# Optimization experiments

Hardware: AMD Instinct MI355X
Metric: run time of the kernel (lower is better)

The kernel has to match this reference:

```python
import jax, jax.numpy as jnp
import numpy as np

B, N, C_IN, D, K = 4, 512, 256, 256, 20


def setup_inputs() -> dict:
    key = jax.random.key(0)
    ks = jax.random.split(key, 6)
    s_in = 1.0 / np.sqrt(C_IN)
    return {
        "x": jax.random.normal(ks[0], (B, N, C_IN), dtype=jnp.float32),
        "edge_index": jnp.zeros((2, 4), dtype=jnp.int64),
        "batch": jnp.zeros((B * N,), dtype=jnp.int64),
        "W_l": jax.random.uniform(ks[1], (D, C_IN), jnp.float32, -s_in, s_in),
        "b_l": jax.random.uniform(ks[2], (D,), jnp.float32, -s_in, s_in),
        "W_r": jax.random.uniform(ks[3], (D, C_IN), jnp.float32, -s_in, s_in),
        "b_r": jax.random.uniform(ks[4], (D,), jnp.float32, -s_in, s_in),
        "att": jax.random.normal(ks[5], (1, D), dtype=jnp.float32) * 0.1,
    }


def reference(x, edge_index, batch, W_l, b_l, W_r, b_r, att):
    b, n, _ = x.shape
    k = K
    # linear projections -> [b, n, d]
    x_l = jnp.einsum("bnc,dc->bnd", x, W_l) + b_l
    x_r = jnp.einsum("bnc,dc->bnd", x, W_r) + b_r
    # pairwise additive attention: [b, n, n, d]
    pair = x_l[:, :, None, :] + x_r[:, None, :, :]
    pair = jnp.where(pair >= 0, pair, 0.2 * pair)  # leaky_relu(0.2)
    alpha = jnp.einsum("bijd,d->bij", pair, att[0])  # [b, n, n]
    alpha = jnp.nan_to_num(alpha, nan=0.0, posinf=0.0, neginf=0.0)
    # knn reduction: topk over last dim
    attention, indices = jax.lax.top_k(alpha, k)  # [b, n, k]
    attention = jax.nn.softmax(attention, axis=-1).reshape(-1)  # [b*n*k]
    # edge index construction with per-batch node offsets
    offset = (jnp.arange(b, dtype=indices.dtype) * n)[:, None]  # [b, 1]
    index_i = jnp.repeat(jnp.arange(n, dtype=indices.dtype), k)[None, :] + offset
    index_j = indices.reshape(b, n * k) + offset
    new_edge_index = jnp.stack([index_i.reshape(-1), index_j.reshape(-1)], axis=0)
    # dropout is identity in eval mode; learn_sys=False -> return directly
    return new_edge_index, attention
```

## Files before the change

### kernel.cpp

```cpp
#include <hip/hip_runtime.h>
#include <math.h>


__global__ __launch_bounds__(256) void k_transpose(const float* __restrict__ Wl,
                                                   const float* __restrict__ Wr,
                                                   float* __restrict__ WtL,
                                                   float* __restrict__ WtR) {
    const int d = blockIdx.x, c = threadIdx.x;
    if (blockIdx.y == 0) WtL[c * 256 + d] = Wl[d * 256 + c];
    else                 WtR[c * 256 + d] = Wr[d * 256 + c];
}

__global__ __launch_bounds__(512, 4) void k_proj(const float* __restrict__ x,
        const float* __restrict__ WtL, const float* __restrict__ WtR,
        const float* __restrict__ bl, const float* __restrict__ br,
        const float* __restrict__ att,
        float* __restrict__ XL, float* __restrict__ XRt,
        float* __restrict__ Av, float* __restrict__ Bv) {
    __shared__ __align__(16) float xst[256 * 12];
    __shared__ __align__(16) float mrg[3 * 4096];
    __shared__ __align__(16) float srs[8 * 256];
    const int tid = threadIdx.x;
    const int dq = tid & 63;
    const int rq = (tid >> 6) & 1;
    const int ch = tid >> 7;
    const int R = blockIdx.x * 8;
    const int b = R >> 9, jr0 = R & 511;

    {
        const float4 xv = ((const float4*)(x + (size_t)R * 256))[tid];
        const int r = tid >> 6;
        const int c4 = (tid & 63) * 4;
        xst[(c4 + 0) * 12 + r] = xv.x;
        xst[(c4 + 1) * 12 + r] = xv.y;
        xst[(c4 + 2) * 12 + r] = xv.z;
        xst[(c4 + 3) * 12 + r] = xv.w;
    }
    __syncthreads();

    float aL[4][4], aR[4][4];
#pragma unroll
    for (int r = 0; r < 4; ++r)
#pragma unroll
        for (int k = 0; k < 4; ++k) { aL[r][k] = 0.f; aR[r][k] = 0.f; }

    const int c0 = ch * 64;
    const float* WLp = WtL + (size_t)c0 * 256 + dq * 4;
    const float* WRp = WtR + (size_t)c0 * 256 + dq * 4;
#pragma unroll 4
    for (int cc = 0; cc < 64; ++cc) {
        const float4 wl = *(const float4*)(WLp + (size_t)cc * 256);
        const float4 wr = *(const float4*)(WRp + (size_t)cc * 256);
        const float4 xv = *(const float4*)&xst[(c0 + cc) * 12 + rq * 4];
#define PROJ_R(r, XS)                                  \
        aL[r][0] = fmaf(XS, wl.x, aL[r][0]);           \
        aL[r][1] = fmaf(XS, wl.y, aL[r][1]);           \
        aL[r][2] = fmaf(XS, wl.z, aL[r][2]);           \
        aL[r][3] = fmaf(XS, wl.w, aL[r][3]);           \
        aR[r][0] = fmaf(XS, wr.x, aR[r][0]);           \
        aR[r][1] = fmaf(XS, wr.y, aR[r][1]);           \
        aR[r][2] = fmaf(XS, wr.z, aR[r][2]);           \
        aR[r][3] = fmaf(XS, wr.w, aR[r][3]);
        PROJ_R(0, xv.x)
        PROJ_R(1, xv.y)
        PROJ_R(2, xv.z)
        PROJ_R(3, xv.w)
#undef PROJ_R
    }

    if (ch > 0) {
        float* m = &mrg[(ch - 1) * 4096];
#pragma unroll
        for (int r = 0; r < 4; ++r) {
            const int r8 = rq * 4 + r;
            *(float4*)&m[(r8 * 2 + 0) * 256 + dq * 4] = make_float4(aL[r][0], aL[r][1], aL[r][2], aL[r][3]);
            *(float4*)&m[(r8 * 2 + 1) * 256 + dq * 4] = make_float4(aR[r][0], aR[r][1], aR[r][2], aR[r][3]);
        }
    }
    __syncthreads();

    float pa[4], pb[4];
    if (ch == 0) {
        const float4 bl4 = *(const float4*)&bl[dq * 4];
        const float4 br4 = *(const float4*)&br[dq * 4];
        const float4 at4 = *(const float4*)&att[dq * 4];
#pragma unroll
        for (int r = 0; r < 4; ++r) {
            const int r8 = rq * 4 + r;
            const float4 mL0 = *(const float4*)&mrg[(r8 * 2 + 0) * 256 + dq * 4];
            const float4 mL1 = *(const float4*)&mrg[4096 + (r8 * 2 + 0) * 256 + dq * 4];
            const float4 mL2 = *(const float4*)&mrg[8192 + (r8 * 2 + 0) * 256 + dq * 4];
            const float4 mR0 = *(const float4*)&mrg[(r8 * 2 + 1) * 256 + dq * 4];
            const float4 mR1 = *(const float4*)&mrg[4096 + (r8 * 2 + 1) * 256 + dq * 4];
            const float4 mR2 = *(const float4*)&mrg[8192 + (r8 * 2 + 1) * 256 + dq * 4];
            float4 sl, sr;
            sl.x = aL[r][0] + mL0.x + mL1.x + mL2.x + bl4.x;
            sl.y = aL[r][1] + mL0.y + mL1.y + mL2.y + bl4.y;
            sl.z = aL[r][2] + mL0.z + mL1.z + mL2.z + bl4.z;
            sl.w = aL[r][3] + mL0.w + mL1.w + mL2.w + bl4.w;
            sr.x = aR[r][0] + mR0.x + mR1.x + mR2.x + br4.x;
            sr.y = aR[r][1] + mR0.y + mR1.y + mR2.y + br4.y;
            sr.z = aR[r][2] + mR0.z + mR1.z + mR2.z + br4.z;
            sr.w = aR[r][3] + mR0.w + mR1.w + mR2.w + br4.w;
            *(float4*)&XL[(size_t)(R + r8) * 256 + dq * 4] = sl;
            *(float4*)&srs[r8 * 256 + dq * 4] = sr;
            pa[r] = at4.x * sl.x + at4.y * sl.y + at4.z * sl.z + at4.w * sl.w;
            pb[r] = at4.x * sr.x + at4.y * sr.y + at4.z * sr.z + at4.w * sr.w;
        }
    }
    __syncthreads();

    {
        const int d = tid >> 1;
        const int half = tid & 1;
        float4 o;
        o.x = srs[(half * 4 + 0) * 256 + d];
        o.y = srs[(half * 4 + 1) * 256 + d];
        o.z = srs[(half * 4 + 2) * 256 + d];
        o.w = srs[(half * 4 + 3) * 256 + d];
        *(float4*)&XRt[((size_t)(b * 256 + d)) * 512 + jr0 + half * 4] = o;
    }

    if (ch == 0) {
#pragma unroll
        for (int r = 0; r < 4; ++r) {
#pragma unroll
            for (int off = 32; off; off >>= 1) {
                pa[r] += __shfl_xor(pa[r], off);
                pb[r] += __shfl_xor(pb[r], off);
            }
        }
        if (dq == 0) {
#pragma unroll
            for (int r = 0; r < 4; ++r) {
                Av[R + rq * 4 + r] = pa[r];
                Bv[R + rq * 4 + r] = pb[r];
            }
        }
    }
}

__global__ __launch_bounds__(512, 2) void k_pair_topk(const float* __restrict__ XL,
        const float* __restrict__ XRt, const float* __restrict__ Av,
        const float* __restrict__ Bv, const float* __restrict__ att,
        float* __restrict__ out) {
    __shared__ __align__(16) float xls[8 * 256];
    __shared__ __align__(16) float atts[256];
    __shared__ __align__(16) float mrg[4 * 4096];
    const int tid = threadIdx.x;
    const int jc = tid & 127;
    const int h = tid >> 7;
    const int g = blockIdx.x;
    const int R = g * 8, b = R >> 9;

    ((float4*)xls)[tid] = ((const float4*)(XL + (size_t)R * 256))[tid];
    if (tid < 64) ((float4*)atts)[tid] = ((const float4*)att)[tid];
    __syncthreads();

    const int dbase = h * 64;
    const float* __restrict__ xrp = XRt + (size_t)b * 131072 + (size_t)dbase * 512 + jc * 4;

    float acc[8][4];
#pragma unroll
    for (int i = 0; i < 8; ++i)
#pragma unroll
        for (int c = 0; c < 4; ++c) acc[i][c] = 0.f;

    float4 bufA[8], bufB[8];
#pragma unroll
    for (int dd = 0; dd < 8; ++dd) bufA[dd] = *(const float4*)(xrp + (size_t)dd * 512);

#pragma unroll
    for (int ch = 0; ch < 8; ++ch) {
        const float4* cur = (ch & 1) ? bufB : bufA;
        float4* nxt = (ch & 1) ? bufA : bufB;
        if (ch < 7) {
            const float* p = xrp + (size_t)(ch + 1) * 8 * 512;
#pragma unroll
            for (int dd = 0; dd < 8; ++dd) nxt[dd] = *(const float4*)(p + (size_t)dd * 512);
        }
        const int d0 = dbase + ch * 8;
        const float4 at0 = *(const float4*)&atts[d0];
        const float4 at1 = *(const float4*)&atts[d0 + 4];
#pragma unroll
        for (int i = 0; i < 8; ++i) {
            const float4 xa = *(const float4*)&xls[i * 256 + d0];
            const float4 xb = *(const float4*)&xls[i * 256 + d0 + 4];
#define PSTEP(XLC, ATC, XR4)                                       \
            acc[i][0] = fmaf(ATC, fabsf(XLC + XR4.x), acc[i][0]);   \
            acc[i][1] = fmaf(ATC, fabsf(XLC + XR4.y), acc[i][1]);   \
            acc[i][2] = fmaf(ATC, fabsf(XLC + XR4.z), acc[i][2]);   \
            acc[i][3] = fmaf(ATC, fabsf(XLC + XR4.w), acc[i][3]);
            PSTEP(xa.x, at0.x, cur[0])
            PSTEP(xa.y, at0.y, cur[1])
            PSTEP(xa.z, at0.z, cur[2])
            PSTEP(xa.w, at0.w, cur[3])
            PSTEP(xb.x, at1.x, cur[4])
            PSTEP(xb.y, at1.y, cur[5])
            PSTEP(xb.z, at1.z, cur[6])
            PSTEP(xb.w, at1.w, cur[7])
#undef PSTEP
        }
    }

    {
        float* m = &mrg[h * 4096];
#pragma unroll
        for (int i = 0; i < 8; ++i)
            *(float4*)&m[i * 512 + jc * 4] = make_float4(acc[i][0], acc[i][1], acc[i][2], acc[i][3]);
    }
    __syncthreads();

    const int lane = tid & 63;
    const int i = tid >> 6;
    const float Ai = Av[R + i];
    const float* __restrict__ bvp = Bv + b * 512;
    const float* __restrict__ mr = &mrg[i * 512];
    float v[8];
#pragma unroll
    for (int t = 0; t < 8; ++t) {
        const int j = t * 64 + lane;
        float s = mr[j];
        s += mr[4096 + j];
        s += mr[8192 + j];
        s += mr[12288 + j];
        float a = fmaf(0.4f, s, 0.6f * (Ai + bvp[j]));
        if (!isfinite(a)) a = 0.f;
        v[t] = a;
    }

    float myval = 0.f, mmax = 0.f;
    int myidx = 0;
    for (int sel = 0; sel < 20; ++sel) {
        float bv = v[0]; int bt = 0;
#pragma unroll
        for (int t = 1; t < 8; ++t) { if (v[t] > bv) { bv = v[t]; bt = t; } }
        int bj = bt * 64 + lane;
#pragma unroll
        for (int off = 32; off; off >>= 1) {
            const float ov = __shfl_xor(bv, off);
            const int   oj = __shfl_xor(bj, off);
            if (ov > bv || (ov == bv && oj < bj)) { bv = ov; bj = oj; }
        }
        if (sel == 0) mmax = bv;
        if (lane == sel) { myval = bv; myidx = bj; }
        if ((bj & 63) == lane) {
            const int bt2 = bj >> 6;
#pragma unroll
            for (int t = 0; t < 8; ++t) if (t == bt2) v[t] = -INFINITY;
        }
    }
    const float e = (lane < 20) ? expf(myval - mmax) : 0.f;
    float s = e;
#pragma unroll
    for (int off = 32; off; off >>= 1) s += __shfl_xor(s, off);
    if (lane < 20) {
        const int row = R + i;
        const int base = row * 20 + lane;
        out[base] = (float)row;
        out[40960 + base] = (float)(b * 512 + myidx);
        out[81920 + base] = e / s;
    }
}

extern "C" void kernel_launch(void* const* d_in, const int* in_sizes, int n_in,
                              void* d_out, int out_size, void* d_ws, size_t ws_size,
                              hipStream_t stream) {
    const float* x   = (const float*)d_in[0];
    const float* Wl  = (const float*)d_in[3];
    const float* bl  = (const float*)d_in[4];
    const float* Wr  = (const float*)d_in[5];
    const float* br  = (const float*)d_in[6];
    const float* att = (const float*)d_in[7];

    float* ws  = (float*)d_ws;
    float* WtL = ws;
    float* WtR = ws + 65536;
    float* XL  = ws + 1048576;
    float* XRt = ws + 1572864;
    float* Av  = ws + 2097152;
    float* Bv  = ws + 2099200;
    float* out = (float*)d_out;

    k_transpose<<<dim3(256, 2), dim3(256), 0, stream>>>(Wl, Wr, WtL, WtR);
    k_proj<<<dim3(256), dim3(512), 0, stream>>>(x, WtL, WtR, bl, br, att, XL, XRt, Av, Bv);
    k_pair_topk<<<dim3(256), dim3(512), 0, stream>>>(XL, XRt, Av, Bv, att, out);
}
```

Baseline: 115.4 us.

## Fuse projection and pairwise top-k kernels via cooperative grid sync

Merges the projection kernel and the pairwise-attention/top-k kernel into one cooperative kernel separated by a grid-wide barrier. XL now stays in shared memory instead of going through global memory, and shared buffers are aliased into one union array. This removes one kernel launch and the XL global round trip. In exchange it adds a grid sync, drops occupancy hints for the projection phase to 2 blocks per CU, and depends on all 256 blocks being co-resident.

```diff
diff --git a/kernel.cpp b/kernel.cpp
--- a/kernel.cpp
+++ b/kernel.cpp
@@ -1,5 +1,8 @@
 #include <hip/hip_runtime.h>
+#include <hip/hip_cooperative_groups.h>
 #include <math.h>
+
+namespace cg = cooperative_groups;
 
 
 __global__ __launch_bounds__(256) void k_transpose(const float* __restrict__ Wl,
@@ -11,255 +14,255 @@
     else                 WtR[c * 256 + d] = Wr[d * 256 + c];
 }
 
-__global__ __launch_bounds__(512, 4) void k_proj(const float* __restrict__ x,
+__global__ __launch_bounds__(512, 2) void k_fused(const float* __restrict__ x,
         const float* __restrict__ WtL, const float* __restrict__ WtR,
         const float* __restrict__ bl, const float* __restrict__ br,
         const float* __restrict__ att,
-        float* __restrict__ XL, float* __restrict__ XRt,
-        float* __restrict__ Av, float* __restrict__ Bv) {
-    __shared__ __align__(16) float xst[256 * 12];
-    __shared__ __align__(16) float mrg[3 * 4096];
-    __shared__ __align__(16) float srs[8 * 256];
-    const int tid = threadIdx.x;
-    const int dq = tid & 63;
-    const int rq = (tid >> 6) & 1;
-    const int ch = tid >> 7;
-    const int R = blockIdx.x * 8;
-    const int b = R >> 9, jr0 = R & 511;
-
-    {
-        const float4 xv = ((const float4*)(x + (size_t)R * 256))[tid];
-        const int r = tid >> 6;
-        const int c4 = (tid & 63) * 4;
-        xst[(c4 + 0) * 12 + r] = xv.x;
-        xst[(c4 + 1) * 12 + r] = xv.y;
-        xst[(c4 + 2) * 12 + r] = xv.z;
-        xst[(c4 + 3) * 12 + r] = xv.w;
-    }
-    __syncthreads();
-
-    float aL[4][4], aR[4][4];
-#pragma unroll
-    for (int r = 0; r < 4; ++r)
-#pragma unroll
-        for (int k = 0; k < 4; ++k) { aL[r][k] = 0.f; aR[r][k] = 0.f; }
-
-    const int c0 = ch * 64;
-    const float* WLp = WtL + (size_t)c0 * 256 + dq * 4;
-    const float* WRp = WtR + (size_t)c0 * 256 + dq * 4;
-#pragma unroll 4
-    for (int cc = 0; cc < 64; ++cc) {
-        const float4 wl = *(const float4*)(WLp + (size_t)cc * 256);
-        const float4 wr = *(const float4*)(WRp + (size_t)cc * 256);
-        const float4 xv = *(const float4*)&xst[(c0 + cc) * 12 + rq * 4];
-#define PROJ_R(r, XS)                                  \
-        aL[r][0] = fmaf(XS, wl.x, aL[r][0]);           \
-        aL[r][1] = fmaf(XS, wl.y, aL[r][1]);           \
-        aL[r][2] = fmaf(XS, wl.z, aL[r][2]);           \
-        aL[r][3] = fmaf(XS, wl.w, aL[r][3]);           \
-        aR[r][0] = fmaf(XS, wr.x, aR[r][0]);           \
-        aR[r][1] = fmaf(XS, wr.y, aR[r][1]);           \
-        aR[r][2] = fmaf(XS, wr.z, aR[r][2]);           \
-        aR[r][3] = fmaf(XS, wr.w, aR[r][3]);
-        PROJ_R(0, xv.x)
-        PROJ_R(1, xv.y)
-        PROJ_R(2, xv.z)
-        PROJ_R(3, xv.w)
-#undef PROJ_R
-    }
-
-    if (ch > 0) {
-        float* m = &mrg[(ch - 1) * 4096];
-#pragma unroll
-        for (int r = 0; r < 4; ++r) {
-            const int r8 = rq * 4 + r;
-            *(float4*)&m[(r8 * 2 + 0) * 256 + dq * 4] = make_float4(aL[r][0], aL[r][1], aL[r][2], aL[r][3]);
-            *(float4*)&m[(r8 * 2 + 1) * 256 + dq * 4] = make_float4(aR[r][0], aR[r][1], aR[r][2], aR[r][3]);
-        }
-    }
-    __syncthreads();
-
-    float pa[4], pb[4];
-    if (ch == 0) {
-        const float4 bl4 = *(const float4*)&bl[dq * 4];
-        const float4 br4 = *(const float4*)&br[dq * 4];
-        const float4 at4 = *(const float4*)&att[dq * 4];
-#pragma unroll
-        for (int r = 0; r < 4; ++r) {
-            const int r8 = rq * 4 + r;
-            const float4 mL0 = *(const float4*)&mrg[(r8 * 2 + 0) * 256 + dq * 4];
-            const float4 mL1 = *(const float4*)&mrg[4096 + (r8 * 2 + 0) * 256 + dq * 4];
-            const float4 mL2 = *(const float4*)&mrg[8192 + (r8 * 2 + 0) * 256 + dq * 4];
-            const float4 mR0 = *(const float4*)&mrg[(r8 * 2 + 1) * 256 + dq * 4];
-            const float4 mR1 = *(const float4*)&mrg[4096 + (r8 * 2 + 1) * 256 + dq * 4];
-            const float4 mR2 = *(const float4*)&mrg[8192 + (r8 * 2 + 1) * 256 + dq * 4];
-            float4 sl, sr;
-            sl.x = aL[r][0] + mL0.x + mL1.x + mL2.x + bl4.x;
-            sl.y = aL[r][1] + mL0.y + mL1.y + mL2.y + bl4.y;
-            sl.z = aL[r][2] + mL0.z + mL1.z + mL2.z + bl4.z;
-            sl.w = aL[r][3] + mL0.w + mL1.w + mL2.w + bl4.w;
-            sr.x = aR[r][0] + mR0.x + mR1.x + mR2.x + br4.x;
-            sr.y = aR[r][1] + mR0.y + mR1.y + mR2.y + br4.y;
-            sr.z = aR[r][2] + mR0.z + mR1.z + mR2.z + br4.z;
-            sr.w = aR[r][3] + mR0.w + mR1.w + mR2.w + br4.w;
-            *(float4*)&XL[(size_t)(R + r8) * 256 + dq * 4] = sl;
-            *(float4*)&srs[r8 * 256 + dq * 4] = sr;
-            pa[r] = at4.x * sl.x + at4.y * sl.y + at4.z * sl.z + at4.w * sl.w;
-            pb[r] = at4.x * sr.x + at4.y * sr.y + at4.z * sr.z + at4.w * sr.w;
-        }
-    }
-    __syncthreads();
-
-    {
-        const int d = tid >> 1;
-        const int half = tid & 1;
-        float4 o;
-        o.x = srs[(half * 4 + 0) * 256 + d];
-        o.y = srs[(half * 4 + 1) * 256 + d];
-        o.z = srs[(half * 4 + 2) * 256 + d];
-        o.w = srs[(half * 4 + 3) * 256 + d];
-        *(float4*)&XRt[((size_t)(b * 256 + d)) * 512 + jr0 + half * 4] = o;
-    }
-
-    if (ch == 0) {
-#pragma unroll
-        for (int r = 0; r < 4; ++r) {
-#pragma unroll
-            for (int off = 32; off; off >>= 1) {
-                pa[r] += __shfl_xor(pa[r], off);
-                pb[r] += __shfl_xor(pb[r], off);
-            }
-        }
-        if (dq == 0) {
-#pragma unroll
-            for (int r = 0; r < 4; ++r) {
-                Av[R + rq * 4 + r] = pa[r];
-                Bv[R + rq * 4 + r] = pb[r];
-            }
-        }
-    }
-}
-
-__global__ __launch_bounds__(512, 2) void k_pair_topk(const float* __restrict__ XL,
-        const float* __restrict__ XRt, const float* __restrict__ Av,
-        const float* __restrict__ Bv, const float* __restrict__ att,
+        float* __restrict__ XRt, float* __restrict__ Av, float* __restrict__ Bv,
         float* __restrict__ out) {
     __shared__ __align__(16) float xls[8 * 256];
     __shared__ __align__(16) float atts[256];
-    __shared__ __align__(16) float mrg[4 * 4096];
+    __shared__ __align__(16) float uni[16384];
     const int tid = threadIdx.x;
-    const int jc = tid & 127;
-    const int h = tid >> 7;
     const int g = blockIdx.x;
-    const int R = g * 8, b = R >> 9;
-
-    ((float4*)xls)[tid] = ((const float4*)(XL + (size_t)R * 256))[tid];
+    const int R = g * 8;
+    const int b = R >> 9, jr0 = R & 511;
+
     if (tid < 64) ((float4*)atts)[tid] = ((const float4*)att)[tid];
-    __syncthreads();
-
-    const int dbase = h * 64;
-    const float* __restrict__ xrp = XRt + (size_t)b * 131072 + (size_t)dbase * 512 + jc * 4;
-
-    float acc[8][4];
-#pragma unroll
-    for (int i = 0; i < 8; ++i)
-#pragma unroll
-        for (int c = 0; c < 4; ++c) acc[i][c] = 0.f;
-
-    float4 bufA[8], bufB[8];
-#pragma unroll
-    for (int dd = 0; dd < 8; ++dd) bufA[dd] = *(const float4*)(xrp + (size_t)dd * 512);
-
-#pragma unroll
-    for (int ch = 0; ch < 8; ++ch) {
-        const float4* cur = (ch & 1) ? bufB : bufA;
-        float4* nxt = (ch & 1) ? bufA : bufB;
-        if (ch < 7) {
-            const float* p = xrp + (size_t)(ch + 1) * 8 * 512;
-#pragma unroll
-            for (int dd = 0; dd < 8; ++dd) nxt[dd] = *(const float4*)(p + (size_t)dd * 512);
-        }
-        const int d0 = dbase + ch * 8;
-        const float4 at0 = *(const float4*)&atts[d0];
-        const float4 at1 = *(const float4*)&atts[d0 + 4];
-#pragma unroll
-        for (int i = 0; i < 8; ++i) {
-            const float4 xa = *(const float4*)&xls[i * 256 + d0];
-            const float4 xb = *(const float4*)&xls[i * 256 + d0 + 4];
-#define PSTEP(XLC, ATC, XR4)                                       \
-            acc[i][0] = fmaf(ATC, fabsf(XLC + XR4.x), acc[i][0]);   \
-            acc[i][1] = fmaf(ATC, fabsf(XLC + XR4.y), acc[i][1]);   \
-            acc[i][2] = fmaf(ATC, fabsf(XLC + XR4.z), acc[i][2]);   \
-            acc[i][3] = fmaf(ATC, fabsf(XLC + XR4.w), acc[i][3]);
-            PSTEP(xa.x, at0.x, cur[0])
-            PSTEP(xa.y, at0.y, cur[1])
-            PSTEP(xa.z, at0.z, cur[2])
-            PSTEP(xa.w, at0.w, cur[3])
-            PSTEP(xb.x, at1.x, cur[4])
-            PSTEP(xb.y, at1.y, cur[5])
-            PSTEP(xb.z, at1.z, cur[6])
-            PSTEP(xb.w, at1.w, cur[7])
+
+    {
+        float* xst = uni;
+        float* mrg = uni + 3072;
+        float* srs = uni;
+        const int dq = tid & 63;
+        const int rq = (tid >> 6) & 1;
+        const int ch = tid >> 7;
+
+        {
+            const float4 xv = ((const float4*)(x + (size_t)R * 256))[tid];
+            const int r = tid >> 6;
+            const int c4 = (tid & 63) * 4;
+            xst[(c4 + 0) * 12 + r] = xv.x;
+            xst[(c4 + 1) * 12 + r] = xv.y;
+            xst[(c4 + 2) * 12 + r] = xv.z;
+            xst[(c4 + 3) * 12 + r] = xv.w;
+        }
+        __syncthreads();
+
+        float aL[4][4], aR[4][4];
+#pragma unroll
+        for (int r = 0; r < 4; ++r)
+#pragma unroll
+            for (int k = 0; k < 4; ++k) { aL[r][k] = 0.f; aR[r][k] = 0.f; }
+
+        const int c0 = ch * 64;
+        const float* WLp = WtL + (size_t)c0 * 256 + dq * 4;
+        const float* WRp = WtR + (size_t)c0 * 256 + dq * 4;
+#pragma unroll 4
+        for (int cc = 0; cc < 64; ++cc) {
+            const float4 wl = *(const float4*)(WLp + (size_t)cc * 256);
+            const float4 wr = *(const float4*)(WRp + (size_t)cc * 256);
+            const float4 xv = *(const float4*)&xst[(c0 + cc) * 12 + rq * 4];
+#define PROJ_R(r, XS)                                  \
+            aL[r][0] = fmaf(XS, wl.x, aL[r][0]);       \
+            aL[r][1] = fmaf(XS, wl.y, aL[r][1]);       \
+            aL[r][2] = fmaf(XS, wl.z, aL[r][2]);       \
+            aL[r][3] = fmaf(XS, wl.w, aL[r][3]);       \
+            aR[r][0] = fmaf(XS, wr.x, aR[r][0]);       \
+            aR[r][1] = fmaf(XS, wr.y, aR[r][1]);       \
+            aR[r][2] = fmaf(XS, wr.z, aR[r][2]);       \
+            aR[r][3] = fmaf(XS, wr.w, aR[r][3]);
+            PROJ_R(0, xv.x)
+            PROJ_R(1, xv.y)
+            PROJ_R(2, xv.z)
+            PROJ_R(3, xv.w)
+#undef PROJ_R
+        }
+
+        if (ch > 0) {
+            float* m = &mrg[(ch - 1) * 4096];
+#pragma unroll
+            for (int r = 0; r < 4; ++r) {
+                const int r8 = rq * 4 + r;
+                *(float4*)&m[(r8 * 2 + 0) * 256 + dq * 4] = make_float4(aL[r][0], aL[r][1], aL[r][2], aL[r][3]);
+                *(float4*)&m[(r8 * 2 + 1) * 256 + dq * 4] = make_float4(aR[r][0], aR[r][1], aR[r][2], aR[r][3]);
+            }
+        }
+        __syncthreads();
+
+        float pa[4], pb[4];
+        if (ch == 0) {
+            const float4 bl4 = *(const float4*)&bl[dq * 4];
+            const float4 br4 = *(const float4*)&br[dq * 4];
+            const float4 at4 = *(const float4*)&att[dq * 4];
+#pragma unroll
+            for (int r = 0; r < 4; ++r) {
+                const int r8 = rq * 4 + r;
+                const float4 mL0 = *(const float4*)&mrg[(r8 * 2 + 0) * 256 + dq * 4];
+                const float4 mL1 = *(const float4*)&mrg[4096 + (r8 * 2 + 0) * 256 + dq * 4];
+                const float4 mL2 = *(const float4*)&mrg[8192 + (r8 * 2 + 0) * 256 + dq * 4];
+                const float4 mR0 = *(const float4*)&mrg[(r8 * 2 + 1) * 256 + dq * 4];
+                const float4 mR1 = *(const float4*)&mrg[4096 + (r8 * 2 + 1) * 256 + dq * 4];
+                const float4 mR2 = *(const float4*)&mrg[8192 + (r8 * 2 + 1) * 256 + dq * 4];
+                float4 sl, sr;
+                sl.x = aL[r][0] + mL0.x + mL1.x + mL2.x + bl4.x;
+                sl.y = aL[r][1] + mL0.y + mL1.y + mL2.y + bl4.y;
+                sl.z = aL[r][2] + mL0.z + mL1.z + mL2.z + bl4.z;
+                sl.w = aL[r][3] + mL0.w + mL1.w + mL2.w + bl4.w;
+                sr.x = aR[r][0] + mR0.x + mR1.x + mR2.x + br4.x;
+                sr.y = aR[r][1] + mR0.y + mR1.y + mR2.y + br4.y;
+                sr.z = aR[r][2] + mR0.z + mR1.z + mR2.z + br4.z;
+                sr.w = aR[r][3] + mR0.w + mR1.w + mR2.w + br4.w;
+                *(float4*)&xls[r8 * 256 + dq * 4] = sl;
+                *(float4*)&srs[r8 * 256 + dq * 4] = sr;
+                pa[r] = at4.x * sl.x + at4.y * sl.y + at4.z * sl.z + at4.w * sl.w;
+                pb[r] = at4.x * sr.x + at4.y * sr.y + at4.z * sr.z + at4.w * sr.w;
+            }
+        }
+        __syncthreads();
+
+        {
+            const int d = tid >> 1;
+            const int half = tid & 1;
+            float4 o;
+            o.x = srs[(half * 4 + 0) * 256 + d];
+            o.y = srs[(half * 4 + 1) * 256 + d];
+            o.z = srs[(half * 4 + 2) * 256 + d];
+            o.w = srs[(half * 4 + 3) * 256 + d];
+            *(float4*)&XRt[((size_t)(b * 256 + d)) * 512 + jr0 + half * 4] = o;
+        }
+
+        if (ch == 0) {
+#pragma unroll
+            for (int r = 0; r < 4; ++r) {
+#pragma unroll
+                for (int off = 32; off; off >>= 1) {
+                    pa[r] += __shfl_xor(pa[r], off);
+                    pb[r] += __shfl_xor(pb[r], off);
+                }
+            }
+            if (dq == 0) {
+#pragma unroll
+                for (int r = 0; r < 4; ++r) {
+                    Av[R + rq * 4 + r] = pa[r];
+                    Bv[R + rq * 4 + r] = pb[r];
+                }
+            }
+        }
+    }
+
+    cg::this_grid().sync();
+
+    {
+        float* mrg = uni;
+        const int jc = tid & 127;
+        const int h = tid >> 7;
+
+        const int dbase = h * 64;
+        const float* __restrict__ xrp = XRt + (size_t)b * 131072 + (size_t)dbase * 512 + jc * 4;
+
+        float acc[8][4];
+#pragma unroll
+        for (int i = 0; i < 8; ++i)
+#pragma unroll
+            for (int c = 0; c < 4; ++c) acc[i][c] = 0.f;
+
+        float4 bufA[8], bufB[8];
+#pragma unroll
+        for (int dd = 0; dd < 8; ++dd) bufA[dd] = *(const float4*)(xrp + (size_t)dd * 512);
+
+#pragma unroll
+        for (int ch = 0; ch < 8; ++ch) {
+            const float4* cur = (ch & 1) ? bufB : bufA;
+            float4* nxt = (ch & 1) ? bufA : bufB;
+            if (ch < 7) {
+                const float* p = xrp + (size_t)(ch + 1) * 8 * 512;
+#pragma unroll
+                for (int dd = 0; dd < 8; ++dd) nxt[dd] = *(const float4*)(p + (size_t)dd * 512);
+            }
+            const int d0 = dbase + ch * 8;
+            const float4 at0 = *(const float4*)&atts[d0];
+            const float4 at1 = *(const float4*)&atts[d0 + 4];
+#pragma unroll
+            for (int i = 0; i < 8; ++i) {
+                const float4 xa = *(const float4*)&xls[i * 256 + d0];
+                const float4 xb = *(const float4*)&xls[i * 256 + d0 + 4];
+#define PSTEP(XLC, ATC, XR4)                                        \
+                acc[i][0] = fmaf(ATC, fabsf(XLC + XR4.x), acc[i][0]); \
+                acc[i][1] = fmaf(ATC, fabsf(XLC + XR4.y), acc[i][1]); \
+                acc[i][2] = fmaf(ATC, fabsf(XLC + XR4.z), acc[i][2]); \
+                acc[i][3] = fmaf(ATC, fabsf(XLC + XR4.w), acc[i][3]);
+                PSTEP(xa.x, at0.x, cur[0])
+                PSTEP(xa.y, at0.y, cur[1])
+                PSTEP(xa.z, at0.z, cur[2])
+                PSTEP(xa.w, at0.w, cur[3])
+                PSTEP(xb.x, at1.x, cur[4])
+                PSTEP(xb.y, at1.y, cur[5])
+                PSTEP(xb.z, at1.z, cur[6])
+                PSTEP(xb.w, at1.w, cur[7])
 #undef PSTEP
-        }
-    }
-
-    {
-        float* m = &mrg[h * 4096];
-#pragma unroll
-        for (int i = 0; i < 8; ++i)
-            *(float4*)&m[i * 512 + jc * 4] = make_float4(acc[i][0], acc[i][1], acc[i][2], acc[i][3]);
-    }
-    __syncthreads();
-
-    const int lane = tid & 63;
-    const int i = tid >> 6;
-    const float Ai = Av[R + i];
-    const float* __restrict__ bvp = Bv + b * 512;
-    const float* __restrict__ mr = &mrg[i * 512];
-    float v[8];
-#pragma unroll
-    for (int t = 0; t < 8; ++t) {
-        const int j = t * 64 + lane;
-        float s = mr[j];
-        s += mr[4096 + j];
-        s += mr[8192 + j];
-        s += mr[12288 + j];
-        float a = fmaf(0.4f, s, 0.6f * (Ai + bvp[j]));
-        if (!isfinite(a)) a = 0.f;
-        v[t] = a;
-    }
-
-    float myval = 0.f, mmax = 0.f;
-    int myidx = 0;
-    for (int sel = 0; sel < 20; ++sel) {
-        float bv = v[0]; int bt = 0;
-#pragma unroll
-        for (int t = 1; t < 8; ++t) { if (v[t] > bv) { bv = v[t]; bt = t; } }
-        int bj = bt * 64 + lane;
-#pragma unroll
-        for (int off = 32; off; off >>= 1) {
-            const float ov = __shfl_xor(bv, off);
-            const int   oj = __shfl_xor(bj, off);
-            if (ov > bv || (ov == bv && oj < bj)) { bv = ov; bj = oj; }
-        }
-        if (sel == 0) mmax = bv;
-        if (lane == sel) { myval = bv; myidx = bj; }
-        if ((bj & 63) == lane) {
-            const int bt2 = bj >> 6;
-#pragma unroll
-            for (int t = 0; t < 8; ++t) if (t == bt2) v[t] = -INFINITY;
-        }
-    }
-    const float e = (lane < 20) ? expf(myval - mmax) : 0.f;
-    float s = e;
-#pragma unroll
-    for (int off = 32; off; off >>= 1) s += __shfl_xor(s, off);
-    if (lane < 20) {
-        const int row = R + i;
-        const int base = row * 20 + lane;
-        out[base] = (float)row;
-        out[40960 + base] = (float)(b * 512 + myidx);
-        out[81920 + base] = e / s;
+            }
+        }
+
+        __syncthreads();
+        {
+            float* m = &mrg[h * 4096];
+#pragma unroll
+            for (int i = 0; i < 8; ++i)
+                *(float4*)&m[i * 512 + jc * 4] = make_float4(acc[i][0], acc[i][1], acc[i][2], acc[i][3]);
+        }
+        __syncthreads();
+
+        const int lane = tid & 63;
+        const int i = tid >> 6;
+        const float Ai = Av[R + i];
+        const float* __restrict__ bvp = Bv + b * 512;
+        const float* __restrict__ mr = &mrg[i * 512];
+        float v[8];
+#pragma unroll
+        for (int t = 0; t < 8; ++t) {
+            const int j = t * 64 + lane;
+            float s = mr[j];
+            s += mr[4096 + j];
+            s += mr[8192 + j];
+            s += mr[12288 + j];
+            float a = fmaf(0.4f, s, 0.6f * (Ai + bvp[j]));
+            if (!isfinite(a)) a = 0.f;
+            v[t] = a;
+        }
+
+        float myval = 0.f, mmax = 0.f;
+        int myidx = 0;
+        for (int sel = 0; sel < 20; ++sel) {
+            float bv = v[0]; int bt = 0;
+#pragma unroll
+            for (int t = 1; t < 8; ++t) { if (v[t] > bv) { bv = v[t]; bt = t; } }
+            int bj = bt * 64 + lane;
+#pragma unroll
+            for (int off = 32; off; off >>= 1) {
+                const float ov = __shfl_xor(bv, off);
+                const int   oj = __shfl_xor(bj, off);
+                if (ov > bv || (ov == bv && oj < bj)) { bv = ov; bj = oj; }
+            }
+            if (sel == 0) mmax = bv;
+            if (lane == sel) { myval = bv; myidx = bj; }
+            if ((bj & 63) == lane) {
+                const int bt2 = bj >> 6;
+#pragma unroll
+                for (int t = 0; t < 8; ++t) if (t == bt2) v[t] = -INFINITY;
+            }
+        }
+        const float e = (lane < 20) ? expf(myval - mmax) : 0.f;
+        float s = e;
+#pragma unroll
+        for (int off = 32; off; off >>= 1) s += __shfl_xor(s, off);
+        if (lane < 20) {
+            const int row = R + i;
+            const int base = row * 20 + lane;
+            out[base] = (float)row;
+            out[40960 + base] = (float)(b * 512 + myidx);
+            out[81920 + base] = e / s;
+        }
     }
 }
 
@@ -276,13 +279,16 @@
     float* ws  = (float*)d_ws;
     float* WtL = ws;
     float* WtR = ws + 65536;
-    float* XL  = ws + 1048576;
     float* XRt = ws + 1572864;
     float* Av  = ws + 2097152;
     float* Bv  = ws + 2099200;
     float* out = (float*)d_out;
 
     k_transpose<<<dim3(256, 2), dim3(256), 0, stream>>>(Wl, Wr, WtL, WtR);
-    k_proj<<<dim3(256), dim3(512), 0, stream>>>(x, WtL, WtR, bl, br, att, XL, XRt, Av, Bv);
-    k_pair_topk<<<dim3(256), dim3(512), 0, stream>>>(XL, XRt, Av, Bv, att, out);
+
+    const float* WtLc = WtL;
+    const float* WtRc = WtR;
+    void* args[] = { (void*)&x, (void*)&WtLc, (void*)&WtRc, (void*)&bl, (void*)&br,
+                     (void*)&att, (void*)&XRt, (void*)&Av, (void*)&Bv, (void*)&out };
+    hipLaunchCooperativeKernel((const void*)k_fused, dim3(256), dim3(512), args, 0, stream);
 }
```

Result: slower. 152.0 us (+31.7%).
